# Kernel optimization log

Measured on AMD Instinct MI355X. Metric: run time of the kernel, lower is better.

The kernel has to match this reference:

```python
import jax, jax.numpy as jnp
import numpy as np

B, T, D, H = 256, 512, 128, 256

def setup_inputs() -> dict:
    key = jax.random.key(0)
    ks = jax.random.split(key, 10)
    s_in = 1.0 / np.sqrt(H + D)
    s_td = 1.0 / np.sqrt(D)
    return {
        "x": jax.random.normal(ks[0], (B, T, D), dtype=jnp.float32),
        "delta": jax.random.uniform(ks[1], (B, T, D), dtype=jnp.float32),
        "W_mu": jax.random.uniform(ks[2], (H + D, H), minval=-s_in, maxval=s_in),
        "b_mu": jax.random.uniform(ks[3], (H,), minval=-s_in, maxval=s_in),
        "W_r": jax.random.uniform(ks[4], (H + D, H), minval=-s_in, maxval=s_in),
        "b_r": jax.random.uniform(ks[5], (H,), minval=-s_in, maxval=s_in),
        "W_h": jax.random.uniform(ks[6], (H + D, H), minval=-s_in, maxval=s_in),
        "b_h": jax.random.uniform(ks[7], (H,), minval=-s_in, maxval=s_in),
        "W_td": jax.random.uniform(ks[8], (D, H), minval=-s_td, maxval=s_td),
        "b_td": jax.random.uniform(ks[9], (H,), minval=-s_td, maxval=s_td),
    }

def reference(x, delta, W_mu, b_mu, W_r, b_r, W_h, b_h, W_td, b_td):
    # GRU-D style GRUI encoder; dropout is identity (eval mode).
    # Precompute temporal decay for all steps at once: beta [B,T,H]
    beta = jnp.exp(-jax.nn.relu(jnp.einsum('btd,dh->bth', delta, W_td) + b_td))
    # Precompute the x-part of the gate GEMMs (W split: first H rows act on h, last D on x)
    Wh_r, Wx_r = W_r[:H], W_r[H:]
    Wh_mu, Wx_mu = W_mu[:H], W_mu[H:]
    Wh_h, Wx_h = W_h[:H], W_h[H:]
    gx_r = jnp.einsum('btd,dh->bth', x, Wx_r) + b_r    # [B,T,H]
    gx_mu = jnp.einsum('btd,dh->bth', x, Wx_mu) + b_mu
    gx_h = jnp.einsum('btd,dh->bth', x, Wx_h) + b_h

    def step(h, inputs):
        beta_t, gxr_t, gxm_t, gxh_t = inputs
        h = beta_t * h
        r_t = jax.nn.sigmoid(h @ Wh_r + gxr_t)
        mu_t = jax.nn.sigmoid(h @ Wh_mu + gxm_t)
        h_hat = jnp.tanh((r_t * h) @ Wh_h + gxh_t)
        h = (1.0 - mu_t) * h + mu_t * h_hat
        return h, None

    h0 = jnp.zeros((x.shape[0], H), dtype=x.dtype)
    seq = (beta.transpose(1, 0, 2), gx_r.transpose(1, 0, 2),
           gx_mu.transpose(1, 0, 2), gx_h.transpose(1, 0, 2))
    h_T, _ = jax.lax.scan(step, h0, seq)
    return h_T
```

## Files before the change

### kernel.cpp

```cpp
#include <hip/hip_runtime.h>
#include <stdint.h>

#define TT 512
#define HB 256
#define DD 128

typedef _Float16 h2_t __attribute__((ext_vector_type(2)));
typedef _Float16 h8_t __attribute__((ext_vector_type(8)));
typedef float    f4_t __attribute__((ext_vector_type(4)));
typedef uint32_t u4_t __attribute__((ext_vector_type(4)));

#define GX_SZ 67108864ull

__device__ __forceinline__ uint32_t pack_h2f(float lo, float hi) {
  h2_t h; h[0] = (_Float16)lo; h[1] = (_Float16)hi;
  return __builtin_bit_cast(uint32_t, h);
}

__device__ __forceinline__ float fdot2f(uint32_t a, uint32_t b, float c) {
#if __has_builtin(__builtin_amdgcn_fdot2)
  return __builtin_amdgcn_fdot2(__builtin_bit_cast(h2_t, a),
                                __builtin_bit_cast(h2_t, b), c, false);
#else
  asm("v_dot2_f32_f16 %0, %1, %2, %0" : "+v"(c) : "v"(a), "v"(b));
  return c;
#endif
}

__device__ __forceinline__ float dpp_xor1(float x) {
  return __builtin_bit_cast(float, __builtin_amdgcn_update_dpp(
      0, __builtin_bit_cast(int, x), 0xB1, 0xF, 0xF, true));
}
__device__ __forceinline__ float dpp_xor2(float x) {
  return __builtin_bit_cast(float, __builtin_amdgcn_update_dpp(
      0, __builtin_bit_cast(int, x), 0x4E, 0xF, 0xF, true));
}
__device__ __forceinline__ float swz_xor4(float x) {
  return __builtin_bit_cast(float, __builtin_amdgcn_ds_swizzle(
      __builtin_bit_cast(int, x), 0x101F));
}

__device__ __forceinline__ void barrier_lds() {
  asm volatile("s_waitcnt lgkmcnt(0)" ::: "memory");
  __builtin_amdgcn_s_barrier();
  __builtin_amdgcn_sched_barrier(0);
}

__global__ __launch_bounds__(256)
void pack_w(const float* __restrict__ Wr, const float* __restrict__ Wmu,
            const float* __restrict__ Wh, const float* __restrict__ Wtd,
            uint8_t* __restrict__ bt) {
  const int id = blockIdx.x * 256 + threadIdx.x;
  const int a = id >> 14, rem = id & 16383;
  const int c = rem >> 6, kp = rem & 63;
  const float* W = (a==0) ? Wr : (a==1) ? Wmu : (a==2) ? Wh : Wtd;
  const int r0 = (a==3) ? 0 : 256;
  const uint32_t v = pack_h2f(W[(r0 + 2*kp)*256 + c], W[(r0 + 2*kp + 1)*256 + c]);
  *(uint32_t*)(bt + a*65536 + c*256 + ((kp*4) ^ ((c & 7) << 4))) = v;
}

__global__ __launch_bounds__(256, 2)
void gemm_pre(const float* __restrict__ x, const float* __restrict__ delta,
              const float* __restrict__ br, const float* __restrict__ bmu,
              const float* __restrict__ bh, const float* __restrict__ btd,
              const uint8_t* __restrict__ bt, uint8_t* __restrict__ ws) {
  __shared__ uint8_t BT[65536];
  const int a  = blockIdx.x & 3;
  const int m0 = (blockIdx.x >> 2) * 128;
  const int tid = threadIdx.x;
  const int l = tid & 63, w = tid >> 6;
  const float* Asrc = (a == 3) ? delta : x;
  const float* bias = (a==0) ? br : (a==1) ? bmu : (a==2) ? bh : btd;

  {
    const u4_t* s4 = (const u4_t*)(bt + (size_t)a*65536);
    u4_t* d4 = (u4_t*)BT;
    #pragma unroll
    for (int i = 0; i < 16; i++) d4[i*256 + tid] = s4[i*256 + tid];
  }
  __syncthreads();

  f4_t acc[2][16];
  #pragma unroll
  for (int rt = 0; rt < 2; rt++)
    #pragma unroll
    for (int nt = 0; nt < 16; nt++) acc[rt][nt] = (f4_t){0.f, 0.f, 0.f, 0.f};

  const int rbase = m0 + w*32 + (l & 15);
  #pragma unroll
  for (int ks = 0; ks < 4; ks++) {
    h8_t af[2];
    #pragma unroll
    for (int rt = 0; rt < 2; rt++) {
      const float* ap = Asrc + (size_t)(rbase + rt*16)*128 + ks*32 + (l >> 4)*8;
      f4_t f0 = *(const f4_t*)ap;
      f4_t f1 = *(const f4_t*)(ap + 4);
      h8_t v;
      v[0]=(_Float16)f0[0]; v[1]=(_Float16)f0[1]; v[2]=(_Float16)f0[2]; v[3]=(_Float16)f0[3];
      v[4]=(_Float16)f1[0]; v[5]=(_Float16)f1[1]; v[6]=(_Float16)f1[2]; v[7]=(_Float16)f1[3];
      af[rt] = v;
    }
    #pragma unroll
    for (int nt = 0; nt < 16; nt++) {
      const int c = nt*16 + (l & 15);
      const int boff = c*256 + ((ks*64 + (l >> 4)*16) ^ ((c & 7) << 4));
      h8_t bf = __builtin_bit_cast(h8_t, *(const u4_t*)(BT + boff));
      acc[0][nt] = __builtin_amdgcn_mfma_f32_16x16x32_f16(af[0], bf, acc[0][nt], 0, 0, 0);
      acc[1][nt] = __builtin_amdgcn_mfma_f32_16x16x32_f16(af[1], bf, acc[1][nt], 0, 0, 0);
    }
  }

  _Float16* outp = (_Float16*)(ws + (size_t)a * GX_SZ);
  #pragma unroll
  for (int nt = 0; nt < 16; nt++) {
    const int c = nt*16 + (l & 15);
    const float bv = bias[c];
    #pragma unroll
    for (int rt = 0; rt < 2; rt++) {
      #pragma unroll
      for (int i = 0; i < 4; i++) {
        const int row = m0 + w*32 + rt*16 + (l >> 4)*4 + i;
        float z = acc[rt][nt][i] + bv;
        if (a == 3) z = __expf(-fmaxf(z, 0.f));
        outp[(size_t)row*256 + c] = (_Float16)z;
      }
    }
  }
}

__global__ __launch_bounds__(512)
__attribute__((amdgpu_waves_per_eu(2, 2)))
void scan_k(const uint8_t* __restrict__ ws,
            const float* __restrict__ Wr, const float* __restrict__ Wmu,
            const float* __restrict__ Wh, float* __restrict__ out) {
  const int b = blockIdx.x;
  const int tid = threadIdx.x;
  const int l = tid & 63, w = tid >> 6;
  const int kq = l & 7, co = l >> 3;
  const int b0 = l & 1, b1 = (l >> 1) & 1, b2 = (l >> 2) & 1;

  __shared__ __align__(16) float hbf[256];
  __shared__ float muv[256];
  __shared__ u4_t  hb4[40];
  __shared__ u4_t  rh4[40];

  const int g = w >> 2;
  const int c1 = (w & 3)*64 + l;
  const int cD = w*32 + co*4 + (l & 3);

  const float* WG = (g == 0) ? Wr : Wmu;
  uint32_t w1b[8][16];
  #pragma unroll
  for (int p = 0; p < 16; p++) {
    const int r0 = kq*32 + 2*p;
    #pragma unroll
    for (int j = 0; j < 8; j++) {
      const int c = (w & 3)*64 + co*8 + j;
      w1b[j][p] = pack_h2f(WG[r0*256 + c], WG[(r0+1)*256 + c]);
    }
  }
  uint32_t w2b[4][16];
  #pragma unroll
  for (int p = 0; p < 16; p++) {
    const int r0 = kq*32 + 2*p;
    #pragma unroll
    for (int j = 0; j < 4; j++) {
      const int c = w*32 + co*4 + j;
      w2b[j][p] = pack_h2f(Wh[r0*256 + c], Wh[(r0+1)*256 + c]);
    }
  }

  if (tid < 40)  hb4[tid] = (u4_t){0, 0, 0, 0};
  if (tid < 256) hbf[tid] = 0.f;

  const uint32_t rowbase = (uint32_t)b * (TT*HB) * 2u;
  const uint32_t gxP1off = (uint32_t)g * (uint32_t)GX_SZ + rowbase + (uint32_t)c1*2u;
  const uint32_t gxhoff  = 2u*(uint32_t)GX_SZ + rowbase + (uint32_t)cD*2u;
  const uint32_t betoff  = 3u*(uint32_t)GX_SZ + rowbase + (uint32_t)(cD & ~1)*2u;

  uint16_t gxA  = *(const uint16_t*)(ws + gxP1off);
  uint16_t gxhA = *(const uint16_t*)(ws + gxhoff);
  uint32_t bA   = *(const uint32_t*)(ws + betoff + 1u*512u);

  __syncthreads();

  #pragma unroll 1
  for (int t = 0; t < TT; t++) {
    const int tn  = (t < TT-1) ? t+1 : TT-1;
    const int tn2 = (t < TT-2) ? t+2 : TT-1;
    uint16_t gxN  = *(const uint16_t*)(ws + gxP1off + (uint32_t)tn*512u);
    uint16_t gxhN = *(const uint16_t*)(ws + gxhoff + (uint32_t)tn*512u);
    uint32_t bN   = *(const uint32_t*)(ws + betoff + (uint32_t)tn2*512u);

    float a8[8] = {0,0,0,0,0,0,0,0};
    #pragma unroll
    for (int q = 0; q < 4; q++) {
      u4_t hp = hb4[kq*5 + q];
      #pragma unroll
      for (int e = 0; e < 4; e++) {
        const uint32_t hv = hp[e];
        #pragma unroll
        for (int j = 0; j < 8; j++) a8[j] = fdot2f(w1b[j][q*4 + e], hv, a8[j]);
      }
    }
    float s4[4];
    #pragma unroll
    for (int j = 0; j < 4; j++) {
      const float keep = b0 ? a8[2*j+1] : a8[2*j];
      const float snd  = b0 ? a8[2*j]   : a8[2*j+1];
      s4[j] = keep + dpp_xor1(snd);
    }
    float s2[2];
    #pragma unroll
    for (int j = 0; j < 2; j++) {
      const float keep = b1 ? s4[2*j+1] : s4[2*j];
      const float snd  = b1 ? s4[2*j]   : s4[2*j+1];
      s2[j] = keep + dpp_xor2(snd);
    }
    {
      const float keep = b2 ? s2[1] : s2[0];
      const float snd  = b2 ? s2[0] : s2[1];
      const float sum = keep + swz_xor4(snd);

      const float z = sum + (float)__builtin_bit_cast(_Float16, gxA);
      const float v = 1.f / (1.f + __expf(-z));
      if (g == 1) {
        muv[c1] = v;
      } else {
        const float vn = dpp_xor1(v);
        const float2 hb2 = *(const float2*)&hbf[c1 & ~1];
        const float rh0 = v  * hb2.x;
        const float rh1 = vn * hb2.y;
        if (b0 == 0) {
          const int pp = c1 >> 1;
          ((uint32_t*)rh4)[(pp >> 4)*20 + (pp & 15)] = pack_h2f(rh0, rh1);
        }
      }
    }
    barrier_lds();

    float d4v[4] = {0,0,0,0};
    #pragma unroll
    for (int q = 0; q < 4; q++) {
      u4_t hp = rh4[kq*5 + q];
      #pragma unroll
      for (int e = 0; e < 4; e++) {
        const uint32_t hv = hp[e];
        #pragma unroll
        for (int j = 0; j < 4; j++) d4v[j] = fdot2f(w2b[j][q*4 + e], hv, d4v[j]);
      }
    }
    float t2[2];
    #pragma unroll
    for (int j = 0; j < 2; j++) {
      const float keep = b0 ? d4v[2*j+1] : d4v[2*j];
      const float snd  = b0 ? d4v[2*j]   : d4v[2*j+1];
      t2[j] = keep + dpp_xor1(snd);
    }
    float t1;
    {
      const float keep = b1 ? t2[1] : t2[0];
      const float snd  = b1 ? t2[0] : t2[1];
      t1 = keep + dpp_xor2(snd);
    }
    const float sum2 = t1 + swz_xor4(t1);

    {
      const float z2 = sum2 + (float)__builtin_bit_cast(_Float16, gxhA);
      const float e2 = __expf(2.f * z2);
      const float hh = 1.f - 2.f / (e2 + 1.f);
      const float hbv = hbf[cD];
      const float hn  = hbv + muv[cD] * (hh - hbv);
      const float vn  = dpp_xor1(hn);
      if ((l & 5) == 0) {
        const h2_t bp = __builtin_bit_cast(h2_t, bA);
        const float hb0 = (float)bp[0] * hn;
        const float hb1 = (float)bp[1] * vn;
        const int pp = cD >> 1;
        ((uint32_t*)hb4)[(pp >> 4)*20 + (pp & 15)] = pack_h2f(hb0, hb1);
        *(float2*)&hbf[cD] = (float2){hb0, hb1};
        if (t == TT-1) *(float2*)(out + b*256 + cD) = (float2){hn, vn};
      }
    }
    gxA = gxN; gxhA = gxhN; bA = bN;
    barrier_lds();
  }
}

extern "C" void kernel_launch(void* const* d_in, const int* in_sizes, int n_in,
                              void* d_out, int out_size, void* d_ws, size_t ws_size,
                              hipStream_t stream) {
  const float* x    = (const float*)d_in[0];
  const float* delta= (const float*)d_in[1];
  const float* Wmu  = (const float*)d_in[2];
  const float* bmu  = (const float*)d_in[3];
  const float* Wr   = (const float*)d_in[4];
  const float* br   = (const float*)d_in[5];
  const float* Wh   = (const float*)d_in[6];
  const float* bh   = (const float*)d_in[7];
  const float* Wtd  = (const float*)d_in[8];
  const float* btd  = (const float*)d_in[9];
  uint8_t* ws = (uint8_t*)d_ws;
  uint8_t* bt = (uint8_t*)d_out;
  float* out = (float*)d_out;

  hipLaunchKernelGGL(pack_w,   dim3(256),  dim3(256), 0, stream, Wr, Wmu, Wh, Wtd, bt);
  hipLaunchKernelGGL(gemm_pre, dim3(4096), dim3(256), 0, stream, x, delta, br, bmu, bh, btd, bt, ws);
  hipLaunchKernelGGL(scan_k,   dim3(256),  dim3(512), 0, stream, ws, Wr, Wmu, Wh, out);
}
```

Baseline: 1.006 ms.

## Double scan block to 1024 threads and halve per-thread weight columns

The recurrent scan kernel now runs 16 waves per batch row instead of 8. Each thread holds half as many weight columns (4 gate and 2 candidate columns), which cuts per-step dot-product work per thread and register pressure. The lane mapping is reworked so that the cross-lane K reduction uses only DPP ops (xor1, xor2, row_shr-style xor8) instead of a ds_swizzle. The cost is more waves taking part in each per-step barrier and more redundant lanes, and occupancy is forced to 4 waves per EU.

Result: slower. 1.261 ms (+25.4%).

```diff
diff --git a/kernel.cpp b/kernel.cpp
--- a/kernel.cpp
+++ b/kernel.cpp
@@ -35,9 +35,9 @@
   return __builtin_bit_cast(float, __builtin_amdgcn_update_dpp(
       0, __builtin_bit_cast(int, x), 0x4E, 0xF, 0xF, true));
 }
-__device__ __forceinline__ float swz_xor4(float x) {
-  return __builtin_bit_cast(float, __builtin_amdgcn_ds_swizzle(
-      __builtin_bit_cast(int, x), 0x101F));
+__device__ __forceinline__ float dpp_xor8(float x) {
+  return __builtin_bit_cast(float, __builtin_amdgcn_update_dpp(
+      0, __builtin_bit_cast(int, x), 0x128, 0xF, 0xF, true));
 }
 
 __device__ __forceinline__ void barrier_lds() {
@@ -128,44 +128,45 @@
   }
 }
 
-__global__ __launch_bounds__(512)
-__attribute__((amdgpu_waves_per_eu(2, 2)))
+__global__ __launch_bounds__(1024)
+__attribute__((amdgpu_waves_per_eu(4, 4)))
 void scan_k(const uint8_t* __restrict__ ws,
             const float* __restrict__ Wr, const float* __restrict__ Wmu,
             const float* __restrict__ Wh, float* __restrict__ out) {
   const int b = blockIdx.x;
   const int tid = threadIdx.x;
   const int l = tid & 63, w = tid >> 6;
-  const int kq = l & 7, co = l >> 3;
-  const int b0 = l & 1, b1 = (l >> 1) & 1, b2 = (l >> 2) & 1;
+  const int co2 = ((l >> 2) & 1) | (((l >> 4) & 3) << 1);
+  const int kq2 = (l & 3) | (((l >> 3) & 1) << 2);
+  const int b0 = l & 1, b1 = (l >> 1) & 1;
 
   __shared__ __align__(16) float hbf[256];
   __shared__ float muv[256];
   __shared__ u4_t  hb4[40];
   __shared__ u4_t  rh4[40];
 
-  const int g = w >> 2;
-  const int c1 = (w & 3)*64 + l;
-  const int cD = w*32 + co*4 + (l & 3);
+  const int g = w >> 3;
+  const int c1 = (w & 7)*32 + co2*4 + (l & 3);
+  const int cD = w*16 + co2*2 + b0;
 
   const float* WG = (g == 0) ? Wr : Wmu;
-  uint32_t w1b[8][16];
+  uint32_t w1b[4][16];
   #pragma unroll
   for (int p = 0; p < 16; p++) {
-    const int r0 = kq*32 + 2*p;
-    #pragma unroll
-    for (int j = 0; j < 8; j++) {
-      const int c = (w & 3)*64 + co*8 + j;
+    const int r0 = kq2*32 + 2*p;
+    #pragma unroll
+    for (int j = 0; j < 4; j++) {
+      const int c = (w & 7)*32 + co2*4 + j;
       w1b[j][p] = pack_h2f(WG[r0*256 + c], WG[(r0+1)*256 + c]);
     }
   }
-  uint32_t w2b[4][16];
+  uint32_t w2b[2][16];
   #pragma unroll
   for (int p = 0; p < 16; p++) {
-    const int r0 = kq*32 + 2*p;
-    #pragma unroll
-    for (int j = 0; j < 4; j++) {
-      const int c = w*32 + co*4 + j;
+    const int r0 = kq2*32 + 2*p;
+    #pragma unroll
+    for (int j = 0; j < 2; j++) {
+      const int c = w*16 + co2*2 + j;
       w2b[j][p] = pack_h2f(Wh[r0*256 + c], Wh[(r0+1)*256 + c]);
     }
   }
@@ -192,46 +193,42 @@
     uint16_t gxhN = *(const uint16_t*)(ws + gxhoff + (uint32_t)tn*512u);
     uint32_t bN   = *(const uint32_t*)(ws + betoff + (uint32_t)tn2*512u);
 
-    float a8[8] = {0,0,0,0,0,0,0,0};
+    float a4[4] = {0,0,0,0};
     #pragma unroll
     for (int q = 0; q < 4; q++) {
-      u4_t hp = hb4[kq*5 + q];
+      u4_t hp = hb4[kq2*5 + q];
       #pragma unroll
       for (int e = 0; e < 4; e++) {
         const uint32_t hv = hp[e];
         #pragma unroll
-        for (int j = 0; j < 8; j++) a8[j] = fdot2f(w1b[j][q*4 + e], hv, a8[j]);
-      }
-    }
-    float s4[4];
-    #pragma unroll
-    for (int j = 0; j < 4; j++) {
-      const float keep = b0 ? a8[2*j+1] : a8[2*j];
-      const float snd  = b0 ? a8[2*j]   : a8[2*j+1];
-      s4[j] = keep + dpp_xor1(snd);
+        for (int j = 0; j < 4; j++) a4[j] = fdot2f(w1b[j][q*4 + e], hv, a4[j]);
+      }
     }
     float s2[2];
     #pragma unroll
     for (int j = 0; j < 2; j++) {
-      const float keep = b1 ? s4[2*j+1] : s4[2*j];
-      const float snd  = b1 ? s4[2*j]   : s4[2*j+1];
-      s2[j] = keep + dpp_xor2(snd);
-    }
+      const float keep = b0 ? a4[2*j+1] : a4[2*j];
+      const float snd  = b0 ? a4[2*j]   : a4[2*j+1];
+      s2[j] = keep + dpp_xor1(snd);
+    }
+    float t1;
     {
-      const float keep = b2 ? s2[1] : s2[0];
-      const float snd  = b2 ? s2[0] : s2[1];
-      const float sum = keep + swz_xor4(snd);
-
+      const float keep = b1 ? s2[1] : s2[0];
+      const float snd  = b1 ? s2[0] : s2[1];
+      t1 = keep + dpp_xor2(snd);
+    }
+    const float sum = t1 + dpp_xor8(t1);
+
+    {
       const float z = sum + (float)__builtin_bit_cast(_Float16, gxA);
       const float v = 1.f / (1.f + __expf(-z));
       if (g == 1) {
-        muv[c1] = v;
+        if ((l & 8) == 0) muv[c1] = v;
       } else {
         const float vn = dpp_xor1(v);
-        const float2 hb2 = *(const float2*)&hbf[c1 & ~1];
-        const float rh0 = v  * hb2.x;
-        const float rh1 = vn * hb2.y;
-        if (b0 == 0) {
+        if ((l & 9) == 0) {
+          const float rh0 = v  * hbf[c1];
+          const float rh1 = vn * hbf[c1 + 1];
           const int pp = c1 >> 1;
           ((uint32_t*)rh4)[(pp >> 4)*20 + (pp & 15)] = pack_h2f(rh0, rh1);
         }
@@ -239,31 +236,25 @@
     }
     barrier_lds();
 
-    float d4v[4] = {0,0,0,0};
+    float d2[2] = {0,0};
     #pragma unroll
     for (int q = 0; q < 4; q++) {
-      u4_t hp = rh4[kq*5 + q];
+      u4_t hp = rh4[kq2*5 + q];
       #pragma unroll
       for (int e = 0; e < 4; e++) {
         const uint32_t hv = hp[e];
         #pragma unroll
-        for (int j = 0; j < 4; j++) d4v[j] = fdot2f(w2b[j][q*4 + e], hv, d4v[j]);
-      }
-    }
-    float t2[2];
-    #pragma unroll
-    for (int j = 0; j < 2; j++) {
-      const float keep = b0 ? d4v[2*j+1] : d4v[2*j];
-      const float snd  = b0 ? d4v[2*j]   : d4v[2*j+1];
-      t2[j] = keep + dpp_xor1(snd);
-    }
-    float t1;
+        for (int j = 0; j < 2; j++) d2[j] = fdot2f(w2b[j][q*4 + e], hv, d2[j]);
+      }
+    }
+    float td;
     {
-      const float keep = b1 ? t2[1] : t2[0];
-      const float snd  = b1 ? t2[0] : t2[1];
-      t1 = keep + dpp_xor2(snd);
-    }
-    const float sum2 = t1 + swz_xor4(t1);
+      const float keep = b0 ? d2[1] : d2[0];
+      const float snd  = b0 ? d2[0] : d2[1];
+      td = keep + dpp_xor1(snd);
+    }
+    const float t2v  = td + dpp_xor2(td);
+    const float sum2 = t2v + dpp_xor8(t2v);
 
     {
       const float z2 = sum2 + (float)__builtin_bit_cast(_Float16, gxhA);
@@ -271,15 +262,15 @@
       const float hh = 1.f - 2.f / (e2 + 1.f);
       const float hbv = hbf[cD];
       const float hn  = hbv + muv[cD] * (hh - hbv);
-      const float vn  = dpp_xor1(hn);
-      if ((l & 5) == 0) {
+      const float hn1 = dpp_xor1(hn);
+      if ((l & 11) == 0) {
         const h2_t bp = __builtin_bit_cast(h2_t, bA);
         const float hb0 = (float)bp[0] * hn;
-        const float hb1 = (float)bp[1] * vn;
+        const float hb1 = (float)bp[1] * hn1;
         const int pp = cD >> 1;
         ((uint32_t*)hb4)[(pp >> 4)*20 + (pp & 15)] = pack_h2f(hb0, hb1);
         *(float2*)&hbf[cD] = (float2){hb0, hb1};
-        if (t == TT-1) *(float2*)(out + b*256 + cD) = (float2){hn, vn};
+        if (t == TT-1) *(float2*)(out + b*256 + cD) = (float2){hn, hn1};
       }
     }
     gxA = gxN; gxhA = gxhN; bA = bN;
@@ -306,5 +297,5 @@
 
   hipLaunchKernelGGL(pack_w,   dim3(256),  dim3(256), 0, stream, Wr, Wmu, Wh, Wtd, bt);
   hipLaunchKernelGGL(gemm_pre, dim3(4096), dim3(256), 0, stream, x, delta, br, bmu, bh, btd, bt, ws);
-  hipLaunchKernelGGL(scan_k,   dim3(256),  dim3(512), 0, stream, ws, Wr, Wmu, Wh, out);
-}
+  hipLaunchKernelGGL(scan_k,   dim3(256),  dim3(1024), 0, stream, ws, Wr, Wmu, Wh, out);
+}
```
